# Kernel tuning notes

Hardware: AMD Instinct MI355X
Metric: run time of the kernel (lower is better)

The kernel has to match this reference:

```python
import jax, jax.numpy as jnp
import numpy as np

H = 768      # hidden_size
NH = 12      # num_heads
HD = H // NH # head_dim = 64


def setup_inputs() -> dict:
    key = jax.random.key(0)
    k1, k2, k3 = jax.random.split(key, 3)
    x = jax.random.normal(k1, (4, 2048, H), dtype=jnp.float32)
    # nn.Linear weights are [out, in]; we store transposed [in, out] for x @ W
    w_qkv = jax.random.normal(k2, (H, 3 * H), dtype=jnp.float32) * (1.0 / np.sqrt(H))
    w_out = jax.random.normal(k3, (H, H), dtype=jnp.float32) * (1.0 / np.sqrt(H))
    return {"x": x, "w_qkv": w_qkv, "w_out": w_out}


def reference(x, w_qkv, w_out):
    B, S, _ = x.shape
    qkv = (x @ w_qkv).reshape(B, S, 3, NH, HD)
    qkv = jnp.transpose(qkv, (2, 0, 3, 1, 4))  # [3, B, NH, S, HD]
    q, k, v = qkv[0], qkv[1], qkv[2]
    scale = 1.0 / np.sqrt(HD)
    scores = jnp.einsum('bhqd,bhkd->bhqk', q, k) * scale  # [B,NH,S,S]
    causal = jnp.tril(jnp.ones((S, S), dtype=bool))
    scores = jnp.where(causal, scores, jnp.finfo(scores.dtype).min)
    attn = jax.nn.softmax(scores, axis=-1)
    out = jnp.einsum('bhqk,bhkd->bhqd', attn, v)          # [B,NH,S,HD]
    out = jnp.transpose(out, (0, 2, 1, 3)).reshape(B, S, H)
    return out @ w_out
```

## Files before the change

kernel.cpp:

```cpp
#include <hip/hip_runtime.h>
#include <type_traits>

#define S_LEN 2048
#define HID   768
#define NHEAD 12
#define HDIM  64
#define BATCH 4

typedef __attribute__((ext_vector_type(4))) float float4v;
typedef __attribute__((ext_vector_type(8))) short short8;
typedef __attribute__((ext_vector_type(4))) short short4v;
typedef __attribute__((ext_vector_type(2))) int int2v;

__device__ __forceinline__ short f2b(float f) {
  unsigned u = __float_as_uint(f);
  u += 0x7fff + ((u >> 16) & 1);
  return (short)(u >> 16);
}

__device__ __forceinline__ unsigned pkbf(float a, float b) {
#if __has_builtin(__builtin_amdgcn_cvt_pk_bf16_f32)
  typedef __attribute__((ext_vector_type(2))) __bf16 bf2;
  bf2 r = __builtin_amdgcn_cvt_pk_bf16_f32(a, b);
  return *(unsigned*)&r;
#else
  return ((unsigned)(unsigned short)f2b(a)) |
         (((unsigned)(unsigned short)f2b(b)) << 16);
#endif
}

__device__ __forceinline__ float fexp2(float x) {
#if __has_builtin(__builtin_amdgcn_exp2f)
  return __builtin_amdgcn_exp2f(x);
#else
  return __expf(x * 0.69314718056f);
#endif
}

__device__ __forceinline__ void g2l16(const short* g, short* l) {
  __builtin_amdgcn_global_load_lds(
      (const __attribute__((address_space(1))) void*)g,
      (__attribute__((address_space(3))) void*)l, 16, 0, 0);
}

__global__ __launch_bounds__(256) void prepass(const float* __restrict__ x,
                                               const float* __restrict__ w_qkv,
                                               const float* __restrict__ w_out,
                                               short* __restrict__ xb,
                                               short* __restrict__ wqkvT,
                                               short* __restrict__ woutT) {
  __shared__ float tile[64][65];
  const int blk = blockIdx.x;
  if (blk < 3072) {
    int i = blk * 2048 + threadIdx.x * 8;
    float4v a = *(const float4v*)&x[i];
    float4v b = *(const float4v*)&x[i + 4];
    short8 o;
#pragma unroll
    for (int j = 0; j < 4; j++) { o[j] = f2b(a[j]); o[j + 4] = f2b(b[j]); }
    *(short8*)&xb[i] = o;
    return;
  }
  const float* W; short* WT; int N_, scaleN, idx;
  if (blk < 3504) { idx = blk - 3072; W = w_qkv; WT = wqkvT; N_ = 3 * HID; scaleN = HID; }
  else            { idx = blk - 3504; W = w_out; WT = woutT; N_ = HID;     scaleN = 0;  }
  const int nblk = N_ / 64;
  const int n0 = (idx % nblk) * 64, k0 = (idx / nblk) * 64;
  const int tx = threadIdx.x & 63, ty = threadIdx.x >> 6;
#pragma unroll
  for (int r = 0; r < 16; r++) {
    int row = r * 4 + ty;
    tile[row][tx] = W[(size_t)(k0 + row) * N_ + n0 + tx];
  }
  __syncthreads();
#pragma unroll
  for (int r = 0; r < 16; r++) {
    int row = r * 4 + ty;
    float sc = (n0 + row < scaleN) ? 0.18033688011f : 1.0f;
    WT[(size_t)(n0 + row) * HID + k0 + tx] = f2b(tile[tx][row] * sc);
  }
}

template <int OUT>
__global__ __launch_bounds__(256) void gemm_bt(const short* __restrict__ A,
                                               const short* __restrict__ Bt,
                                               float* __restrict__ Cf,
                                               short* __restrict__ Cq,
                                               short* __restrict__ vT,
                                               int M, int N, int K) {
  __shared__ __align__(16) short As[2][128 * 32];
  __shared__ __align__(16) short Bs[2][128 * 32];
  const int tid = threadIdx.x;
  const int w = tid >> 6, lane = tid & 63;
  const int quad = lane >> 4, lm = lane & 15;
  const int m0 = blockIdx.y * 128, n0 = blockIdx.x * 128;
  const int mo = (w & 1) * 64, no = (w >> 1) * 64;

  float4v acc[4][4];
#pragma unroll
  for (int i = 0; i < 4; i++)
#pragma unroll
    for (int j = 0; j < 4; j++) acc[i][j] = (float4v)0.0f;

  const int srow = w * 32 + (lane >> 2);
  const int scol = (lane & 3) * 8;
  const short* Ag = A + (size_t)(m0 + srow) * K + scol;
  const short* Bg = Bt + (size_t)(n0 + srow) * K + scol;

  for (int kb = 0; kb < K; kb += 64) {
#pragma unroll
    for (int s = 0; s < 2; s++) {
      short* Al = &As[s][(w * 32) * 32];
      short* Bl = &Bs[s][(w * 32) * 32];
      g2l16(Ag + kb + s * 32, Al);
      g2l16(Ag + kb + s * 32 + (size_t)16 * K, Al + 16 * 32);
      g2l16(Bg + kb + s * 32, Bl);
      g2l16(Bg + kb + s * 32 + (size_t)16 * K, Bl + 16 * 32);
    }
    __syncthreads();

#pragma unroll
    for (int s = 0; s < 2; s++) {
      short8 af[4], bf[4];
#pragma unroll
      for (int i = 0; i < 4; i++)
        af[i] = *(const short8*)&As[s][(mo + i * 16 + lm) * 32 + quad * 8];
#pragma unroll
      for (int j = 0; j < 4; j++)
        bf[j] = *(const short8*)&Bs[s][(no + j * 16 + lm) * 32 + quad * 8];
#pragma unroll
      for (int i = 0; i < 4; i++)
#pragma unroll
        for (int j = 0; j < 4; j++)
          acc[i][j] = __builtin_amdgcn_mfma_f32_16x16x32_bf16(af[i], bf[j], acc[i][j], 0, 0, 0);
    }
    __syncthreads();
  }

  if constexpr (OUT == 0) {
#pragma unroll
    for (int i = 0; i < 4; i++)
#pragma unroll
      for (int j = 0; j < 4; j++)
#pragma unroll
        for (int r = 0; r < 4; r++)
          Cf[(size_t)(m0 + mo + i * 16 + quad * 4 + r) * N + n0 + no + j * 16 + lm] =
              acc[i][j][r];
  } else {
    if (n0 >= 2 * HID) {
      const int b = m0 >> 11;
      const int s0 = (m0 & 2047) + mo + quad * 4;
#pragma unroll
      for (int i = 0; i < 4; i++)
#pragma unroll
        for (int j = 0; j < 4; j++) {
          int col = n0 + no + j * 16 + lm - 2 * HID;
          int h = col >> 6, d = col & 63;
          short4v pv;
#pragma unroll
          for (int r = 0; r < 4; r++) pv[r] = f2b(acc[i][j][r]);
          *(short4v*)&vT[((size_t)(b * NHEAD + h) * HDIM + d) * S_LEN + s0 + i * 16] = pv;
        }
    } else {
#pragma unroll
      for (int i = 0; i < 4; i++)
#pragma unroll
        for (int j = 0; j < 4; j++)
#pragma unroll
          for (int r = 0; r < 4; r++)
            Cq[(size_t)(m0 + mo + i * 16 + quad * 4 + r) * (2 * HID) + n0 + no + j * 16 + lm] =
                f2b(acc[i][j][r]);
    }
  }
}

#define PST 72

__global__ __launch_bounds__(256) void attn_mfma(const short* __restrict__ qk,
                                                 const short* __restrict__ vT,
                                                 short* __restrict__ attnout) {
  __shared__ __align__(16) short Qs[128 * PST];
  __shared__ __align__(16) short Ks[64 * PST];
  __shared__ __align__(16) short Vt[64 * PST];
  __shared__ __align__(16) short Ps[4][16 * PST];

  const int tid = threadIdx.x;
  const int w = tid >> 6, lane = tid & 63;
  const int quad = lane >> 4, lm = lane & 15;
  const int bh = blockIdx.x, a = blockIdx.y;
  const int b = bh / NHEAD, h = bh % NHEAD;
  const int qtile[2] = {a, 31 - a};

  const size_t kbase = (size_t)(b * S_LEN) * (2 * HID) + HID + h * HDIM;
  const size_t vbase = (size_t)(b * NHEAD + h) * HDIM * S_LEN;

#pragma unroll
  for (int i = 0; i < 4; i++) {
    int flat = i * 256 + tid;
    int row = flat >> 3, c8 = (flat & 7) * 8;
    int grow = qtile[row >> 6] * 64 + (row & 63);
    *(short8*)&Qs[row * PST + c8] =
        *(const short8*)&qk[(size_t)(b * S_LEN + grow) * (2 * HID) + h * HDIM + c8];
  }

  float4v o_acc[2][4];
#pragma unroll
  for (int t = 0; t < 2; t++)
#pragma unroll
    for (int nt = 0; nt < 4; nt++) o_acc[t][nt] = (float4v)0.0f;
  float lsum[2][4];
#pragma unroll
  for (int t = 0; t < 2; t++)
#pragma unroll
    for (int r = 0; r < 4; r++) lsum[t][r] = 0.0f;

  const int ktmax = 32 - a;
  short8 kreg[2], vreg[2];

#define PREFETCH(KT)                                                               \
  {                                                                                \
    _Pragma("unroll") for (int i = 0; i < 2; i++) {                                \
      int flat = i * 256 + tid;                                                    \
      int p = flat >> 3, c8 = (flat & 7) * 8;                                      \
      int key = 4 * (p & 15) + (p >> 4);                                           \
      kreg[i] = *(const short8*)&qk[kbase + (size_t)((KT)*64 + key) * (2*HID) + c8]; \
      vreg[i] = *(const short8*)&vT[vbase + (size_t)p * S_LEN + (KT)*64 + c8];     \
    }                                                                              \
  }

  PREFETCH(0);

  for (int kt = 0; kt < ktmax; kt++) {
    __syncthreads();
#pragma unroll
    for (int i = 0; i < 2; i++) {
      int flat = i * 256 + tid;
      int p = flat >> 3, c8 = (flat & 7) * 8;
      *(short8*)&Ks[p * PST + c8] = kreg[i];
      *(short8*)&Vt[p * PST + c8] = vreg[i];
    }
    __syncthreads();
    if (kt + 1 < ktmax) PREFETCH(kt + 1);

#pragma unroll
    for (int t = 0; t < 2; t++) {
      if (t == 0 && kt > a) continue;
      float4v s_acc[4];
#pragma unroll
      for (int i = 0; i < 4; i++) s_acc[i] = (float4v)0.0f;
#pragma unroll
      for (int kb = 0; kb < 2; kb++) {
        short8 aq = *(const short8*)&Qs[(t * 64 + w * 16 + lm) * PST + kb * 32 + quad * 8];
#pragma unroll
        for (int nt = 0; nt < 4; nt++) {
          short8 bk = *(const short8*)&Ks[(nt * 16 + lm) * PST + kb * 32 + quad * 8];
          s_acc[nt] = __builtin_amdgcn_mfma_f32_16x16x32_bf16(aq, bk, s_acc[nt], 0, 0, 0);
        }
      }

      const bool diag = (kt == qtile[t]);
#pragma unroll
      for (int r = 0; r < 4; r++) {
        float e[4];
#pragma unroll
        for (int nt = 0; nt < 4; nt++) {
          float v = fexp2(s_acc[nt][r]);
          if (diag && (4 * lm + nt > w * 16 + quad * 4 + r)) v = 0.0f;
          lsum[t][r] += v;
          e[nt] = v;
        }
        int2v p2 = {(int)pkbf(e[0], e[1]), (int)pkbf(e[2], e[3])};
        *(int2v*)&Ps[w][(quad * 4 + r) * PST + lm * 4] = p2;
      }

#pragma unroll
      for (int kb = 0; kb < 2; kb++) {
        short8 ap = *(const short8*)&Ps[w][lm * PST + kb * 32 + quad * 8];
#pragma unroll
        for (int nt = 0; nt < 4; nt++) {
          short8 bv = *(const short8*)&Vt[(nt * 16 + lm) * PST + kb * 32 + quad * 8];
          o_acc[t][nt] = __builtin_amdgcn_mfma_f32_16x16x32_bf16(ap, bv, o_acc[t][nt], 0, 0, 0);
        }
      }
    }
  }

#pragma unroll
  for (int t = 0; t < 2; t++)
#pragma unroll
    for (int r = 0; r < 4; r++) {
#pragma unroll
      for (int off = 1; off < 16; off <<= 1)
        lsum[t][r] += __shfl_xor(lsum[t][r], off, 16);
      float inv = 1.0f / lsum[t][r];
      int rowg = b * S_LEN + qtile[t] * 64 + w * 16 + quad * 4 + r;
#pragma unroll
      for (int nt = 0; nt < 4; nt++)
        attnout[(size_t)rowg * HID + h * HDIM + nt * 16 + lm] =
            f2b(o_acc[t][nt][r] * inv);
    }
}

extern "C" void kernel_launch(void* const* d_in, const int* in_sizes, int n_in,
                              void* d_out, int out_size, void* d_ws, size_t ws_size,
                              hipStream_t stream) {
  const float* x     = (const float*)d_in[0];
  const float* w_qkv = (const float*)d_in[1];
  const float* w_out = (const float*)d_in[2];
  float* out = (float*)d_out;

  const int M = BATCH * S_LEN;
  short* qk     = (short*)d_ws;
  short* attn   = qk + (size_t)M * 2 * HID;
  short* vT     = attn + (size_t)M * HID;
  short* xb     = vT + (size_t)M * HID;
  short* wqkvT  = xb + (size_t)M * HID;
  short* woutT  = wqkvT + (size_t)(3 * HID) * HID;

  prepass<<<3648, 256, 0, stream>>>(x, w_qkv, w_out, xb, wqkvT, woutT);

  gemm_bt<1><<<dim3(3 * HID / 128, M / 128), 256, 0, stream>>>(
      xb, wqkvT, nullptr, qk, vT, M, 3 * HID, HID);
  attn_mfma<<<dim3(BATCH * NHEAD, S_LEN / 128), 256, 0, stream>>>(qk, vT, attn);
  gemm_bt<0><<<dim3(HID / 128, M / 128), 256, 0, stream>>>(
      attn, woutT, out, nullptr, nullptr, M, HID, HID);
}
```

Before: 201.1 us.

## Double-buffer K/V via direct global-to-LDS loads with XOR-swizzled layout

The attention kernel now loads K and V tiles straight from global memory into LDS through a g2l16 helper, using two alternating buffers, so the register staging and the second barrier per iteration go away. Q fragments are kept in registers instead of being staged in shared memory. LDS tiles switch from padded rows to an XOR-swizzled unpadded layout to avoid bank conflicts. In exchange it relies on a full vmcnt(0) wait each iteration and on the g2l16 helper defined elsewhere, and the swizzle indexing must match the load pattern exactly.

Result: no change. 200.6 us (-0.3%).

```diff
diff --git a/kernel.cpp b/kernel.cpp
--- a/kernel.cpp
+++ b/kernel.cpp
@@ -174,15 +174,12 @@
   }
 }
 
-#define PST 72
-
 __global__ __launch_bounds__(256) void attn_mfma(const short* __restrict__ qk,
                                                  const short* __restrict__ vT,
                                                  short* __restrict__ attnout) {
-  __shared__ __align__(16) short Qs[128 * PST];
-  __shared__ __align__(16) short Ks[64 * PST];
-  __shared__ __align__(16) short Vt[64 * PST];
-  __shared__ __align__(16) short Ps[4][16 * PST];
+  __shared__ __align__(16) short Ks[2][64 * 64];
+  __shared__ __align__(16) short Vt[2][64 * 64];
+  __shared__ __align__(16) short Ps[4][16 * 64];
 
   const int tid = threadIdx.x;
   const int w = tid >> 6, lane = tid & 63;
@@ -191,16 +188,34 @@
   const int b = bh / NHEAD, h = bh % NHEAD;
   const int qtile[2] = {a, 31 - a};
 
+  short8 aq[2][2];
+#pragma unroll
+  for (int t = 0; t < 2; t++)
+#pragma unroll
+    for (int kb = 0; kb < 2; kb++)
+      aq[t][kb] = *(const short8*)&qk[(size_t)(b * S_LEN + qtile[t] * 64 + w * 16 + lm) * (2 * HID) +
+                                      h * HDIM + kb * 32 + quad * 8];
+
   const size_t kbase = (size_t)(b * S_LEN) * (2 * HID) + HID + h * HDIM;
   const size_t vbase = (size_t)(b * NHEAD + h) * HDIM * S_LEN;
-
-#pragma unroll
-  for (int i = 0; i < 4; i++) {
-    int flat = i * 256 + tid;
-    int row = flat >> 3, c8 = (flat & 7) * 8;
-    int grow = qtile[row >> 6] * 64 + (row & 63);
-    *(short8*)&Qs[row * PST + c8] =
-        *(const short8*)&qk[(size_t)(b * S_LEN + grow) * (2 * HID) + h * HDIM + c8];
+  const short* ksrc[2];
+  const short* vsrc[2];
+#pragma unroll
+  for (int i = 0; i < 2; i++) {
+    int c = (w * 2 + i) * 64 + lane;
+    int row = c >> 3, slot = c & 7;
+    int q8 = slot ^ (row & 7);
+    int key = 4 * (row & 15) + (row >> 4);
+    ksrc[i] = qk + kbase + (size_t)key * (2 * HID) + q8 * 8;
+    vsrc[i] = vT + vbase + (size_t)row * S_LEN + q8 * 8;
+  }
+
+#define ISSUE(KT, BUF)                                                              \
+  {                                                                                 \
+    _Pragma("unroll") for (int i = 0; i < 2; i++) {                                 \
+      g2l16(ksrc[i] + (size_t)(KT) * 64 * (2 * HID), &Ks[BUF][(w * 2 + i) * 512]);  \
+      g2l16(vsrc[i] + (KT) * 64, &Vt[BUF][(w * 2 + i) * 512]);                      \
+    }                                                                               \
   }
 
   float4v o_acc[2][4];
@@ -215,32 +230,15 @@
     for (int r = 0; r < 4; r++) lsum[t][r] = 0.0f;
 
   const int ktmax = 32 - a;
-  short8 kreg[2], vreg[2];
-
-#define PREFETCH(KT)                                                               \
-  {                                                                                \
-    _Pragma("unroll") for (int i = 0; i < 2; i++) {                                \
-      int flat = i * 256 + tid;                                                    \
-      int p = flat >> 3, c8 = (flat & 7) * 8;                                      \
-      int key = 4 * (p & 15) + (p >> 4);                                           \
-      kreg[i] = *(const short8*)&qk[kbase + (size_t)((KT)*64 + key) * (2*HID) + c8]; \
-      vreg[i] = *(const short8*)&vT[vbase + (size_t)p * S_LEN + (KT)*64 + c8];     \
-    }                                                                              \
-  }
-
-  PREFETCH(0);
+  const int swx = (lm & 7) << 4;
+  int cur = 0;
+
+  ISSUE(0, 0);
 
   for (int kt = 0; kt < ktmax; kt++) {
+    asm volatile("s_waitcnt vmcnt(0)" ::: "memory");
     __syncthreads();
-#pragma unroll
-    for (int i = 0; i < 2; i++) {
-      int flat = i * 256 + tid;
-      int p = flat >> 3, c8 = (flat & 7) * 8;
-      *(short8*)&Ks[p * PST + c8] = kreg[i];
-      *(short8*)&Vt[p * PST + c8] = vreg[i];
-    }
-    __syncthreads();
-    if (kt + 1 < ktmax) PREFETCH(kt + 1);
+    if (kt + 1 < ktmax) ISSUE(kt + 1, cur ^ 1);
 
 #pragma unroll
     for (int t = 0; t < 2; t++) {
@@ -250,11 +248,11 @@
       for (int i = 0; i < 4; i++) s_acc[i] = (float4v)0.0f;
 #pragma unroll
       for (int kb = 0; kb < 2; kb++) {
-        short8 aq = *(const short8*)&Qs[(t * 64 + w * 16 + lm) * PST + kb * 32 + quad * 8];
 #pragma unroll
         for (int nt = 0; nt < 4; nt++) {
-          short8 bk = *(const short8*)&Ks[(nt * 16 + lm) * PST + kb * 32 + quad * 8];
-          s_acc[nt] = __builtin_amdgcn_mfma_f32_16x16x32_bf16(aq, bk, s_acc[nt], 0, 0, 0);
+          short8 bk = *(const short8*)((const char*)&Ks[cur][0] +
+                        ((nt * 16 + lm) << 7) + (((kb * 64 + quad * 16)) ^ swx));
+          s_acc[nt] = __builtin_amdgcn_mfma_f32_16x16x32_bf16(aq[t][kb], bk, s_acc[nt], 0, 0, 0);
         }
       }
 
@@ -270,19 +268,23 @@
           e[nt] = v;
         }
         int2v p2 = {(int)pkbf(e[0], e[1]), (int)pkbf(e[2], e[3])};
-        *(int2v*)&Ps[w][(quad * 4 + r) * PST + lm * 4] = p2;
+        int rowp = quad * 4 + r;
+        *(int2v*)((char*)&Ps[w][0] + (rowp << 7) + ((lm * 8) ^ ((rowp & 7) << 4))) = p2;
       }
 
 #pragma unroll
       for (int kb = 0; kb < 2; kb++) {
-        short8 ap = *(const short8*)&Ps[w][lm * PST + kb * 32 + quad * 8];
+        short8 ap = *(const short8*)((const char*)&Ps[w][0] +
+                      (lm << 7) + ((kb * 64 + quad * 16) ^ swx));
 #pragma unroll
         for (int nt = 0; nt < 4; nt++) {
-          short8 bv = *(const short8*)&Vt[(nt * 16 + lm) * PST + kb * 32 + quad * 8];
+          short8 bv = *(const short8*)((const char*)&Vt[cur][0] +
+                        ((nt * 16 + lm) << 7) + ((kb * 64 + quad * 16) ^ swx));
           o_acc[t][nt] = __builtin_amdgcn_mfma_f32_16x16x32_bf16(ap, bv, o_acc[t][nt], 0, 0, 0);
         }
       }
     }
+    cur ^= 1;
   }
 
 #pragma unroll
@@ -299,6 +301,7 @@
         attnout[(size_t)rowg * HID + h * HDIM + nt * 16 + lm] =
             f2b(o_acc[t][nt][r] * inv);
     }
+#undef ISSUE
 }
 
 extern "C" void kernel_launch(void* const* d_in, const int* in_sizes, int n_in,
```
